# Performance work log

Hardware: AMD Instinct MI355X
Metric: run time of the kernel (lower is better)

Reference implementation:

```python
import jax, jax.numpy as jnp
import numpy as np

B, T = 256, 64
L, S = 1024, 512          # large / small LSTM cell sizes
NC = 239                  # num classes
EPS = 1e-5                # BatchNorm eps (inference mode, mean=0, var=1)
TAU = 1.0                 # gumbel-softmax temperature


def setup_inputs() -> dict:
    key = jax.random.key(0)
    ks = jax.random.split(key, 12)
    def N(i, shape, s=0.05):
        return jax.random.normal(ks[i], shape, dtype=jnp.float32) * s
    return {
        "x": N(0, (B, T, 2048), 1.0),
        "x_small": N(1, (B, T, 1280), 1.0),
        # proj_mlp: Linear(2048->2048) + BN(2048) [inference] + ReLU
        "W_p": N(2, (2048, 2048)), "b_p": jnp.zeros(2048),
        "g_p": jnp.ones(2048), "be_p": jnp.zeros(2048),
        # small_proj_mlp: Linear(1280->512) + BN(512) + ReLU
        "W_s": N(3, (512, 1280)), "b_s": jnp.zeros(512),
        "g_s": jnp.ones(512), "be_s": jnp.zeros(512),
        # large LSTMCell: input 2048+512 -> hidden L
        "Wih_l": N(4, (4 * L, 2048 + 512)), "Whh_l": N(5, (4 * L, L)),
        "bih_l": jnp.zeros(4 * L), "bhh_l": jnp.zeros(4 * L),
        # small LSTMCell: input 512 -> hidden S
        "Wih_s": N(6, (4 * S, 512)), "Whh_s": N(7, (4 * S, S)),
        "bih_s": jnp.zeros(4 * S), "bhh_s": jnp.zeros(4 * S),
        # gate linear: (512 + 2L) -> 2
        "W_g": N(8, (2, 512 + 2 * L)), "b_g": jnp.zeros(2),
        # classifier: L -> NC
        "W_c": N(9, (NC, L)), "b_c": jnp.zeros(NC),
    }


def _bn_relu(x, gamma, beta):
    # inference BatchNorm1d with running_mean=0, running_var=1
    return jax.nn.relu(x * (gamma / np.sqrt(1.0 + EPS)) + beta)


def _lstm_cell(xin, h, c, Wih, Whh, bih, bhh):
    gates = xin @ Wih.T + bih + h @ Whh.T + bhh
    i, f, g, o = jnp.split(gates, 4, axis=1)
    c2 = jax.nn.sigmoid(f) * c + jax.nn.sigmoid(i) * jnp.tanh(g)
    h2 = jax.nn.sigmoid(o) * jnp.tanh(c2)
    return h2, c2


def reference(x, x_small, W_p, b_p, g_p, be_p, W_s, b_s, g_s, be_s,
              Wih_l, Whh_l, bih_l, bhh_l, Wih_s, Whh_s, bih_s, bhh_s,
              W_g, b_g, W_c, b_c):
    # project all frames at once (time-parallel part of the net)
    feats = _bn_relu(jnp.einsum('bti,oi->bto', x, W_p) + b_p, g_p, be_p)        # [B,T,2048]
    sfeats = _bn_relu(jnp.einsum('bti,oi->bto', x_small, W_s) + b_s, g_s, be_s)  # [B,T,512]

    def step(carry, ft_st):
        h_l, c_l, h_s, c_s = carry
        f_t, s_t = ft_st                                   # [B,2048], [B,512]
        h_s2, c_s2 = _lstm_cell(s_t, h_s, c_s, Wih_s, Whh_s, bih_s, bhh_s)
        # gating on OLD large state
        p = jax.nn.log_softmax(jnp.concatenate([s_t, h_l, c_l], 1) @ W_g.T + b_g, axis=1)
        y_soft = jax.nn.softmax(p / TAU, axis=1)
        y_hard = jax.nn.one_hot(jnp.argmax(y_soft, axis=1), 2, dtype=y_soft.dtype)
        r = y_hard + y_soft - jax.lax.stop_gradient(y_soft)  # straight-through hard sample
        h_ln, c_ln = _lstm_cell(jnp.concatenate([f_t, s_t], 1), h_l, c_l,
                                Wih_l, Whh_l, bih_l, bhh_l)
        ph = jnp.concatenate([h_s2[:, :S], h_l[:, S:L]], 1)  # partial (skip) hidden
        pc = jnp.concatenate([c_s2[:, :S], c_l[:, S:L]], 1)
        h_l2 = r[:, 0:1] * h_ln + r[:, 1:2] * ph
        c_l2 = r[:, 0:1] * c_ln + r[:, 1:2] * pc
        return (h_l2, c_l2, h_s2, c_s2), r

    z_l = jnp.zeros((B, L), jnp.float32)
    z_s = jnp.zeros((B, S), jnp.float32)
    (h_l, c_l, _, _), r_stack = jax.lax.scan(
        step, (z_l, z_l, z_s, z_s),
        (feats.transpose(1, 0, 2), sfeats.transpose(1, 0, 2)))
    logits = h_l @ W_c.T + b_c                             # [B,NC]
    return logits, r_stack                                 # r_stack: [T,B,2]
```

## Files before the change

### kernel.cpp

```cpp
#include <hip/hip_runtime.h>
#include <math.h>


typedef _Float16 f16;
typedef _Float16 f16x4 __attribute__((ext_vector_type(4)));
typedef _Float16 f16x8 __attribute__((ext_vector_type(8)));
typedef float f32x4 __attribute__((ext_vector_type(4)));

__device__ __forceinline__ float sigf(float x) { return 1.0f / (1.0f + expf(-x)); }

__device__ __forceinline__ void gload16(const f16* g, f16* l) {
  __builtin_amdgcn_global_load_lds((const __attribute__((address_space(1))) void*)g,
                                   (__attribute__((address_space(3))) void*)l, 16, 0, 0);
}

__global__ __launch_bounds__(256) void pack_img(const float* __restrict__ src,
    int C, int KT, int t0, int map, f16* __restrict__ dh, f16* __restrict__ dl,
    int slots)
{
  int gid = blockIdx.x * 256 + threadIdx.x;
  if (gid >= slots) return;
  int lane = gid & 63;
  int j = (gid >> 6) & 7;
  int pk = gid >> 9;
  int p = pk / KT, kt = pk - p * KT;
  int r = p * 128 + j * 16 + (lane & 15);
  int rg = map ? (((r & 255) << 6) + t0 + (r >> 8)) : r;
  int c = kt * 32 + (lane >> 4) * 8;
  const float* s = src + (long long)rg * C + c;
  float4 v0 = *(const float4*)s, v1 = *(const float4*)(s + 4);
  f16x8 h, l;
  h[0]=(f16)v0.x; l[0]=(f16)(v0.x-(float)h[0]);
  h[1]=(f16)v0.y; l[1]=(f16)(v0.y-(float)h[1]);
  h[2]=(f16)v0.z; l[2]=(f16)(v0.z-(float)h[2]);
  h[3]=(f16)v0.w; l[3]=(f16)(v0.w-(float)h[3]);
  h[4]=(f16)v1.x; l[4]=(f16)(v1.x-(float)h[4]);
  h[5]=(f16)v1.y; l[5]=(f16)(v1.y-(float)h[5]);
  h[6]=(f16)v1.z; l[6]=(f16)(v1.z-(float)h[6]);
  h[7]=(f16)v1.w; l[7]=(f16)(v1.w-(float)h[7]);
  *(f16x8*)(dh + (long long)gid * 8) = h;
  *(f16x8*)(dl + (long long)gid * 8) = l;
}

template <int EPI>
__global__ __launch_bounds__(512, 1) void gmm256(
    const f16* __restrict__ Ah0, const f16* __restrict__ Al0, int KT0,
    const f16* __restrict__ Ah1, const f16* __restrict__ Al1, int KT1,
    const f16* __restrict__ Bh, const f16* __restrict__ Bl, int KTB,
    float* __restrict__ C, int ldc,
    f16* __restrict__ Ch, f16* __restrict__ Cl, int KTout,
    const float* __restrict__ e0, const float* __restrict__ e1,
    const float* __restrict__ e2)
{
  __shared__ __align__(16) char smem[131072];
  f16 (*sm)[4][8192] = (f16 (*)[4][8192])smem;
  const int tid = threadIdx.x;
  const int w = tid >> 6, lane = tid & 63;
  const int wr = w >> 2, wc = w & 3;
  const int fr = lane & 15, fq = lane >> 4;
  const int pA = blockIdx.y, pB = blockIdx.x;
  const int sarr = w >> 1, shalf = w & 1;

  const int nt = KT0 + KT1;

  auto stage = [&](int buf, int kt) {
    const f16* base;
    if (sarr >= 2) {
      base = ((sarr == 2) ? Bh : Bl) + ((long long)(pB * 2 + shalf) * KTB + kt) * 4096;
    } else if (kt < KT0) {
      base = ((sarr == 0) ? Ah0 : Al0) + ((long long)(pA * 2 + shalf) * KT0 + kt) * 4096;
    } else {
      base = ((sarr == 0) ? Ah1 : Al1) + ((long long)(pA * 2 + shalf) * KT1 + (kt - KT0)) * 4096;
    }
    f16* dst = &sm[buf][sarr][shalf * 4096];
#pragma unroll
    for (int j = 0; j < 8; ++j)
      gload16(base + j * 512 + lane * 8, dst + j * 512);
  };

  f32x4 acc[8][4];
#pragma unroll
  for (int m = 0; m < 8; ++m)
#pragma unroll
    for (int n = 0; n < 4; ++n) acc[m][n] = (f32x4){0.f, 0.f, 0.f, 0.f};

  stage(0, 0);
  __syncthreads();
  int cur = 0;
  for (int kt = 0; kt < nt; ++kt) {
    if (kt + 1 < nt) stage(cur ^ 1, kt + 1);
    f16x8 bh_[4], bl_[4];
#pragma unroll
    for (int n = 0; n < 4; ++n) {
      bh_[n] = *(const f16x8*)&sm[cur][2][(wc * 4 + n) * 512 + lane * 8];
      bl_[n] = *(const f16x8*)&sm[cur][3][(wc * 4 + n) * 512 + lane * 8];
    }
#pragma unroll
    for (int m = 0; m < 8; ++m) {
      f16x8 ah = *(const f16x8*)&sm[cur][0][wr * 4096 + m * 512 + lane * 8];
      f16x8 al = *(const f16x8*)&sm[cur][1][wr * 4096 + m * 512 + lane * 8];
#pragma unroll
      for (int n = 0; n < 4; ++n) {
        acc[m][n] = __builtin_amdgcn_mfma_f32_16x16x32_f16(ah, bh_[n], acc[m][n], 0, 0, 0);
        acc[m][n] = __builtin_amdgcn_mfma_f32_16x16x32_f16(ah, bl_[n], acc[m][n], 0, 0, 0);
        acc[m][n] = __builtin_amdgcn_mfma_f32_16x16x32_f16(al, bh_[n], acc[m][n], 0, 0, 0);
      }
    }
    __syncthreads();
    cur ^= 1;
  }

  if (EPI == 1) {
#pragma unroll
    for (int m = 0; m < 8; ++m) {
#pragma unroll
      for (int n = 0; n < 4; ++n) {
        const int col = pB * 256 + wc * 64 + n * 16 + fr;
        const float add = e0[col] + e1[col];
#pragma unroll
        for (int r = 0; r < 4; ++r) {
          const int row = pA * 256 + wr * 128 + m * 16 + fq * 4 + r;
          C[(long long)row * ldc + col] = acc[m][n][r] + add;
        }
      }
    }
  } else {
    float* cb = (float*)smem;
    const int CBLD = 260;
    for (int q = 0; q < 4; ++q) {
      __syncthreads();
      if (wr == (q >> 1)) {
#pragma unroll
        for (int mm = 0; mm < 4; ++mm) {
          const int m = (q & 1) * 4 + mm;
#pragma unroll
          for (int n = 0; n < 4; ++n) {
            const int colL = wc * 64 + n * 16 + fr;
            const int colG = pB * 256 + colL;
            const float p0 = e0[colG], p1 = e1[colG] * 0.99999500003750f, p2 = e2[colG];
#pragma unroll
            for (int r = 0; r < 4; ++r) {
              const int rq = mm * 16 + fq * 4 + r;
              cb[rq * CBLD + colL] = fmaxf((acc[m][n][r] + p0) * p1 + p2, 0.f);
            }
          }
        }
      }
      __syncthreads();
      const int ktl = w;
      const int p_out = pA * 2 + (q >> 1);
#pragma unroll
      for (int jp = 0; jp < 4; ++jp) {
        const int rL = jp * 16 + fr;
        const float* s = &cb[rL * CBLD + ktl * 32 + fq * 8];
        float4 v0 = *(const float4*)s, v1 = *(const float4*)(s + 4);
        float vv[8] = {v0.x, v0.y, v0.z, v0.w, v1.x, v1.y, v1.z, v1.w};
        f16x8 h, l;
#pragma unroll
        for (int e = 0; e < 8; ++e) {
          h[e] = (f16)vv[e]; l[e] = (f16)(vv[e] - (float)h[e]);
        }
        const int j_img = (q & 1) * 4 + jp;
        const long long o =
            (((long long)p_out * KTout + (pB * 8 + ktl)) * 8 + j_img) * 512 + lane * 8;
        *(f16x8*)(Ch + o) = h;
        *(f16x8*)(Cl + o) = l;
      }
    }
  }
}

__device__ __forceinline__ void gcore_step(int pA, int pB,
    const f16* __restrict__ Ah0, const f16* __restrict__ Al0, int KT0,
    const f16* __restrict__ Bh, const f16* __restrict__ Bl,
    float* __restrict__ C, int ldc, const float* __restrict__ G)
{
  __shared__ __align__(16) char smem[65536];
  f16 (*sm)[4][4096] = (f16 (*)[4][4096])smem;
  const int tid = threadIdx.x;
  const int w = tid >> 6, lane = tid & 63;
  const int wr = w >> 1, wc = w & 1;
  const int fr = lane & 15, fq = lane >> 4;

  const f16* aH = Ah0 + (long long)pA * KT0 * 4096;
  const f16* aL = Al0 + (long long)pA * KT0 * 4096;
  const f16* bH = Bh + (long long)pB * KT0 * 4096;
  const f16* bL = Bl + (long long)pB * KT0 * 4096;

  auto stage = [&](int buf, int kt) {
    const f16* src;
    if (w == 0)      src = aH + (long long)kt * 4096;
    else if (w == 1) src = aL + (long long)kt * 4096;
    else if (w == 2) src = bH + (long long)kt * 4096;
    else             src = bL + (long long)kt * 4096;
    f16* dst = &sm[buf][w][0];
#pragma unroll
    for (int j = 0; j < 8; ++j)
      gload16(src + j * 512 + lane * 8, dst + j * 512);
  };

  f32x4 acc[4][4];
#pragma unroll
  for (int m = 0; m < 4; ++m)
#pragma unroll
    for (int n = 0; n < 4; ++n) acc[m][n] = (f32x4){0.f, 0.f, 0.f, 0.f};

  stage(0, 0);
  __syncthreads();
  int cur = 0;
  for (int kt = 0; kt < KT0; ++kt) {
    if (kt + 1 < KT0) stage(cur ^ 1, kt + 1);
    f16x8 bhx[4], blx[4];
#pragma unroll
    for (int n = 0; n < 4; ++n) {
      bhx[n] = *(const f16x8*)&sm[cur][2][(wc * 4 + n) * 512 + lane * 8];
      blx[n] = *(const f16x8*)&sm[cur][3][(wc * 4 + n) * 512 + lane * 8];
    }
#pragma unroll
    for (int m = 0; m < 4; ++m) {
      f16x8 ah = *(const f16x8*)&sm[cur][0][(wr * 4 + m) * 512 + lane * 8];
      f16x8 al = *(const f16x8*)&sm[cur][1][(wr * 4 + m) * 512 + lane * 8];
#pragma unroll
      for (int n = 0; n < 4; ++n) {
        acc[m][n] = __builtin_amdgcn_mfma_f32_16x16x32_f16(ah, bhx[n], acc[m][n], 0, 0, 0);
        acc[m][n] = __builtin_amdgcn_mfma_f32_16x16x32_f16(ah, blx[n], acc[m][n], 0, 0, 0);
        acc[m][n] = __builtin_amdgcn_mfma_f32_16x16x32_f16(al, bhx[n], acc[m][n], 0, 0, 0);
      }
    }
    __syncthreads();
    cur ^= 1;
  }

#pragma unroll
  for (int m = 0; m < 4; ++m) {
#pragma unroll
    for (int n = 0; n < 4; ++n) {
      const int col = pB * 128 + wc * 64 + n * 16 + fr;
#pragma unroll
      for (int r = 0; r < 4; ++r) {
        const int row = pA * 128 + wr * 64 + m * 16 + fq * 4 + r;
        const long long idx = (long long)row * ldc + col;
        C[idx] = acc[m][n][r] + G[idx];
      }
    }
  }
}

__global__ __launch_bounds__(256) void stepg_k(
    const f16* __restrict__ hlh, const f16* __restrict__ hll,
    const f16* __restrict__ hsh, const f16* __restrict__ hsl,
    const f16* __restrict__ Whl_h, const f16* __restrict__ Whl_l,
    const f16* __restrict__ Whs_h, const f16* __restrict__ Whs_l,
    const float* __restrict__ Gl, const float* __restrict__ Gs,
    float* __restrict__ gl, float* __restrict__ gs)
{
  if (blockIdx.y < 32)
    gcore_step(blockIdx.x, blockIdx.y, hlh, hll, 32,
               Whl_h, Whl_l, gl, 4096, Gl);
  else
    gcore_step(blockIdx.x, blockIdx.y - 32, hsh, hsl, 16,
               Whs_h, Whs_l, gs, 2048, Gs);
}

__global__ __launch_bounds__(256) void zs_img_k(const f16* __restrict__ sfh,
    const f16* __restrict__ sfl, const float* __restrict__ Wg,
    float* __restrict__ zs, int t0)
{
  const int wv = threadIdx.x >> 6, lane = threadIdx.x & 63;
  const int rr = blockIdx.x * 4 + wv;
  const int p = rr >> 7, j = (rr >> 4) & 7, fr = rr & 15;
  const int kt = lane >> 2, fq = lane & 3;
  const long long a = (((long long)p * 16 + kt) * 8 + j) * 512 + (fq * 16 + fr) * 8;
  f16x8 h8 = *(const f16x8*)(sfh + a);
  f16x8 l8 = *(const f16x8*)(sfl + a);
  const int k0 = kt * 32 + fq * 8;
  float z0 = 0.f, z1 = 0.f;
#pragma unroll
  for (int i = 0; i < 8; ++i) {
    float s = (float)h8[i] + (float)l8[i];
    z0 += s * Wg[k0 + i]; z1 += s * Wg[2560 + k0 + i];
  }
#pragma unroll
  for (int off = 32; off > 0; off >>= 1) {
    z0 += __shfl_down(z0, off);
    z1 += __shfl_down(z1, off);
  }
  if (lane == 0) {
    const int bt = ((rr & 255) << 6) + t0 + (rr >> 8);
    zs[bt * 2] = z0; zs[bt * 2 + 1] = z1;
  }
}

__global__ __launch_bounds__(256) void step_upd(
    const float* __restrict__ gl, const float* __restrict__ gs,
    const float* __restrict__ hl_o, const float* __restrict__ cl_o,
    const float* __restrict__ cs_o,
    float* __restrict__ hl_n, float* __restrict__ cl_n,
    float* __restrict__ hs_n, float* __restrict__ cs_n,
    f16* __restrict__ hlIh, f16* __restrict__ hlIl,
    f16* __restrict__ hsIh, f16* __restrict__ hsIl,
    const float* __restrict__ zs, const float* __restrict__ Wg,
    const float* __restrict__ bg, float* __restrict__ rout, int t)
{
  const int b = blockIdx.x, tid = threadIdx.x;
  __shared__ float red0[256], red1[256];
  __shared__ float shs[512], scs[512];
  __shared__ float rsh[2];

  const int pb = b >> 7, jb = (b >> 4) & 7, frb = b & 15;

  float4 h4 = *(const float4*)(hl_o + (long long)b * 1024 + tid * 4);
  float4 c4 = *(const float4*)(cl_o + (long long)b * 1024 + tid * 4);
  float4 w0h = *(const float4*)(Wg + 512 + tid * 4);
  float4 w0c = *(const float4*)(Wg + 1536 + tid * 4);
  float4 w1h = *(const float4*)(Wg + 2560 + 512 + tid * 4);
  float4 w1c = *(const float4*)(Wg + 2560 + 1536 + tid * 4);
  red0[tid] = h4.x * w0h.x + h4.y * w0h.y + h4.z * w0h.z + h4.w * w0h.w
            + c4.x * w0c.x + c4.y * w0c.y + c4.z * w0c.z + c4.w * w0c.w;
  red1[tid] = h4.x * w1h.x + h4.y * w1h.y + h4.z * w1h.z + h4.w * w1h.w
            + c4.x * w1c.x + c4.y * w1c.y + c4.z * w1c.z + c4.w * w1c.w;

  {
    const float* gb = gs + (long long)b * 2048;
#pragma unroll
    for (int e = 0; e < 2; ++e) {
      const int n = tid * 2 + e;
      float gi = gb[n], gf = gb[512 + n], gg = gb[1024 + n], go = gb[1536 + n];
      float c2 = sigf(gf) * cs_o[b * 512 + n] + sigf(gi) * tanhf(gg);
      float h2 = sigf(go) * tanhf(c2);
      shs[n] = h2; scs[n] = c2;
      hs_n[b * 512 + n] = h2; cs_n[b * 512 + n] = c2;
      const int kt = n >> 5, fqn = (n >> 3) & 3, en = n & 7;
      const long long o = (((long long)pb * 16 + kt) * 8 + jb) * 512
                        + (fqn * 16 + frb) * 8 + en;
      f16 hh = (f16)h2;
      hsIh[o] = hh; hsIl[o] = (f16)(h2 - (float)hh);
    }
  }
  __syncthreads();
  for (int s = 128; s > 0; s >>= 1) {
    if (tid < s) { red0[tid] += red0[tid + s]; red1[tid] += red1[tid + s]; }
    __syncthreads();
  }
  if (tid == 0) {
    float z0 = red0[0] + zs[(b * 64 + t) * 2 + 0] + bg[0];
    float z1 = red1[0] + zs[(b * 64 + t) * 2 + 1] + bg[1];
    int hard = (z1 > z0) ? 1 : 0;
    rsh[0] = hard ? 0.0f : 1.0f; rsh[1] = hard ? 1.0f : 0.0f;
    rout[b * 2 + 0] = rsh[0]; rout[b * 2 + 1] = rsh[1];
  }
  __syncthreads();
  const float r0 = rsh[0], r1 = rsh[1];

  {
    const float* glb = gl + (long long)b * 4096;
    const int n = tid * 4;
    float4 gi4 = *(const float4*)(glb + n);
    float4 gf4 = *(const float4*)(glb + 1024 + n);
    float4 gg4 = *(const float4*)(glb + 2048 + n);
    float4 go4 = *(const float4*)(glb + 3072 + n);
    float4 co4 = *(const float4*)(cl_o + (long long)b * 1024 + n);
    float4 ho4 = *(const float4*)(hl_o + (long long)b * 1024 + n);
    float gi[4] = {gi4.x, gi4.y, gi4.z, gi4.w};
    float gf[4] = {gf4.x, gf4.y, gf4.z, gf4.w};
    float gg[4] = {gg4.x, gg4.y, gg4.z, gg4.w};
    float go[4] = {go4.x, go4.y, go4.z, go4.w};
    float co[4] = {co4.x, co4.y, co4.z, co4.w};
    float ho[4] = {ho4.x, ho4.y, ho4.z, ho4.w};
    float hv[4], cv[4];
    f16x4 ih, il;
#pragma unroll
    for (int e = 0; e < 4; ++e) {
      float cln = sigf(gf[e]) * co[e] + sigf(gi[e]) * tanhf(gg[e]);
      float hln = sigf(go[e]) * tanhf(cln);
      float ph = (n + e < 512) ? shs[n + e] : ho[e];
      float pc = (n + e < 512) ? scs[n + e] : co[e];
      hv[e] = r0 * hln + r1 * ph;
      cv[e] = r0 * cln + r1 * pc;
      ih[e] = (f16)hv[e]; il[e] = (f16)(hv[e] - (float)ih[e]);
    }
    float4 hw = {hv[0], hv[1], hv[2], hv[3]};
    float4 cw = {cv[0], cv[1], cv[2], cv[3]};
    *(float4*)(hl_n + (long long)b * 1024 + n) = hw;
    *(float4*)(cl_n + (long long)b * 1024 + n) = cw;
    const int kt = n >> 5, fqn = (n >> 3) & 3, en = n & 7;
    const long long o = (((long long)pb * 32 + kt) * 8 + jb) * 512
                      + (fqn * 16 + frb) * 8 + en;
    *(f16x4*)(hlIh + o) = ih;
    *(f16x4*)(hlIl + o) = il;
  }
}

__global__ __launch_bounds__(256) void logits_k(const float* __restrict__ hl,
                                                const float* __restrict__ Wc,
                                                const float* __restrict__ bc,
                                                float* __restrict__ out)
{
  __shared__ float hsd[1024];
  const int b = blockIdx.x, tid = threadIdx.x;
  *(float4*)(hsd + tid * 4) = *(const float4*)(hl + (long long)b * 1024 + tid * 4);
  __syncthreads();
  if (tid < 239) {
    const float* w = Wc + (long long)tid * 1024;
    float s = 0.0f;
    for (int k = 0; k < 1024; k += 4) {
      float4 wv = *(const float4*)(w + k);
      s += hsd[k] * wv.x + hsd[k + 1] * wv.y + hsd[k + 2] * wv.z + hsd[k + 3] * wv.w;
    }
    out[(long long)b * 239 + tid] = s + bc[tid];
  }
}

#define BKK 32
template <int BM, int BN, int TM, int TN, int EPI>
__global__ __launch_bounds__(256) void gemm_nt(
    int M, int N,
    const float* __restrict__ A0, long long as0, const float* __restrict__ B0, long long bs0, int K0,
    const float* __restrict__ A1, long long as1, const float* __restrict__ B1, long long bs1, int K1,
    const float* __restrict__ A2, long long as2, const float* __restrict__ B2, long long bs2, int K2,
    float* __restrict__ C, long long ldc,
    const float* __restrict__ e0, const float* __restrict__ e1, const float* __restrict__ e2)
{
  __shared__ float As[BKK][BM + 4];
  __shared__ float Bs[BKK][BN + 4];
  const int tid = threadIdx.x;
  const int m0 = blockIdx.x * BM;
  const int n0 = blockIdx.y * BN;
  constexpr int C4 = BKK / 4;
  constexpr int RPP = 256 / C4;
  constexpr int APASS = BM / RPP;
  constexpr int BPASS = BN / RPP;
  const int lr = tid / C4;
  const int lc = tid % C4;
  float4 pa[APASS], pb[BPASS];
  const int nt = (K0 + K1 + K2) / BKK;
  auto load = [&](int kt) {
    const int kg = kt * BKK;
    const float* ap; long long as_; const float* bp; long long bs_;
    if (kg < K0)           { ap = A0 + kg;          as_ = as0; bp = B0 + kg;          bs_ = bs0; }
    else if (kg < K0 + K1) { int kl = kg - K0;      ap = A1 + kl; as_ = as1; bp = B1 + kl; bs_ = bs1; }
    else                   { int kl = kg - K0 - K1; ap = A2 + kl; as_ = as2; bp = B2 + kl; bs_ = bs2; }
#pragma unroll
    for (int p = 0; p < APASS; p++) {
      int r = lr + p * RPP;
      pa[p] = *(const float4*)(ap + (long long)(m0 + r) * as_ + lc * 4);
    }
#pragma unroll
    for (int p = 0; p < BPASS; p++) {
      int r = lr + p * RPP;
      pb[p] = *(const float4*)(bp + (long long)(n0 + r) * bs_ + lc * 4);
    }
  };
  const int tx = tid % (BN / TN);
  const int ty = tid / (BN / TN);
  float acc[TM][TN];
#pragma unroll
  for (int i = 0; i < TM; i++)
#pragma unroll
    for (int j = 0; j < TN; j++) acc[i][j] = 0.0f;
  load(0);
  for (int kt = 0; kt < nt; ++kt) {
    __syncthreads();
#pragma unroll
    for (int p = 0; p < APASS; p++) {
      int r = lr + p * RPP;
      As[lc * 4 + 0][r] = pa[p].x; As[lc * 4 + 1][r] = pa[p].y;
      As[lc * 4 + 2][r] = pa[p].z; As[lc * 4 + 3][r] = pa[p].w;
    }
#pragma unroll
    for (int p = 0; p < BPASS; p++) {
      int r = lr + p * RPP;
      Bs[lc * 4 + 0][r] = pb[p].x; Bs[lc * 4 + 1][r] = pb[p].y;
      Bs[lc * 4 + 2][r] = pb[p].z; Bs[lc * 4 + 3][r] = pb[p].w;
    }
    __syncthreads();
    if (kt + 1 < nt) load(kt + 1);
#pragma unroll
    for (int k = 0; k < BKK; k++) {
      float a[TM], bfr[TN];
#pragma unroll
      for (int i = 0; i < TM; i++) a[i] = As[k][ty * TM + i];
#pragma unroll
      for (int j = 0; j < TN; j++) bfr[j] = Bs[k][tx * TN + j];
#pragma unroll
      for (int i = 0; i < TM; i++)
#pragma unroll
        for (int j = 0; j < TN; j++) acc[i][j] += a[i] * bfr[j];
    }
  }
#pragma unroll
  for (int i = 0; i < TM; i++) {
    const int m = m0 + ty * TM + i;
    const int n = n0 + tx * TN;
    float v[TN];
#pragma unroll
    for (int j = 0; j < TN; j++) {
      float a = acc[i][j];
      if (EPI == 0) {
        float s = e1[n + j] * 0.999995f;
        a = (a + e0[n + j]) * s + e2[n + j];
        a = fmaxf(a, 0.0f);
      } else {
        a = a + e0[n + j] + e1[n + j];
      }
      v[j] = a;
    }
    float4 o; o.x = v[0]; o.y = v[1]; o.z = v[2]; o.w = v[3];
    *(float4*)(C + (long long)m * ldc + n) = o;
  }
}

__global__ __launch_bounds__(256) void zs32_k(const float* __restrict__ sf,
                                              const float* __restrict__ Wg,
                                              float* __restrict__ zs)
{
  const int wave = threadIdx.x >> 6, lane = threadIdx.x & 63;
  const int row = blockIdx.x * 4 + wave;
  const float* s = sf + (long long)row * 512 + lane * 8;
  const float* w0 = Wg + lane * 8;
  const float* w1 = Wg + 2560 + lane * 8;
  float4 sa = *(const float4*)s, sb = *(const float4*)(s + 4);
  float4 a0 = *(const float4*)w0, b0 = *(const float4*)(w0 + 4);
  float4 a1 = *(const float4*)w1, b1 = *(const float4*)(w1 + 4);
  float z0 = sa.x * a0.x + sa.y * a0.y + sa.z * a0.z + sa.w * a0.w
           + sb.x * b0.x + sb.y * b0.y + sb.z * b0.z + sb.w * b0.w;
  float z1 = sa.x * a1.x + sa.y * a1.y + sa.z * a1.z + sa.w * a1.w
           + sb.x * b1.x + sb.y * b1.y + sb.z * b1.z + sb.w * b1.w;
#pragma unroll
  for (int off = 32; off > 0; off >>= 1) {
    z0 += __shfl_down(z0, off);
    z1 += __shfl_down(z1, off);
  }
  if (lane == 0) { zs[row * 2] = z0; zs[row * 2 + 1] = z1; }
}

__global__ __launch_bounds__(256) void step_upd32(
    const float* __restrict__ gl, const float* __restrict__ gs,
    const float* __restrict__ hl_o, const float* __restrict__ cl_o,
    const float* __restrict__ cs_o,
    float* __restrict__ hl_n, float* __restrict__ cl_n,
    float* __restrict__ hs_n, float* __restrict__ cs_n,
    const float* __restrict__ zs, const float* __restrict__ Wg,
    const float* __restrict__ bg, float* __restrict__ rout, int t)
{
  const int b = blockIdx.x, tid = threadIdx.x;
  __shared__ float red0[256], red1[256];
  __shared__ float shs[512], scs[512];
  __shared__ float rsh[2];
  float4 h4 = *(const float4*)(hl_o + (long long)b * 1024 + tid * 4);
  float4 c4 = *(const float4*)(cl_o + (long long)b * 1024 + tid * 4);
  float4 w0h = *(const float4*)(Wg + 512 + tid * 4);
  float4 w0c = *(const float4*)(Wg + 1536 + tid * 4);
  float4 w1h = *(const float4*)(Wg + 2560 + 512 + tid * 4);
  float4 w1c = *(const float4*)(Wg + 2560 + 1536 + tid * 4);
  red0[tid] = h4.x * w0h.x + h4.y * w0h.y + h4.z * w0h.z + h4.w * w0h.w
            + c4.x * w0c.x + c4.y * w0c.y + c4.z * w0c.z + c4.w * w0c.w;
  red1[tid] = h4.x * w1h.x + h4.y * w1h.y + h4.z * w1h.z + h4.w * w1h.w
            + c4.x * w1c.x + c4.y * w1c.y + c4.z * w1c.z + c4.w * w1c.w;
  {
    const float* gb = gs + (long long)b * 2048;
#pragma unroll
    for (int e = 0; e < 2; ++e) {
      const int n = tid * 2 + e;
      float gi = gb[n], gf = gb[512 + n], gg = gb[1024 + n], go = gb[1536 + n];
      float c2 = sigf(gf) * cs_o[b * 512 + n] + sigf(gi) * tanhf(gg);
      float h2 = sigf(go) * tanhf(c2);
      shs[n] = h2; scs[n] = c2;
      hs_n[b * 512 + n] = h2; cs_n[b * 512 + n] = c2;
    }
  }
  __syncthreads();
  for (int s = 128; s > 0; s >>= 1) {
    if (tid < s) { red0[tid] += red0[tid + s]; red1[tid] += red1[tid + s]; }
    __syncthreads();
  }
  if (tid == 0) {
    float z0 = red0[0] + zs[(b * 64 + t) * 2 + 0] + bg[0];
    float z1 = red1[0] + zs[(b * 64 + t) * 2 + 1] + bg[1];
    int hard = (z1 > z0) ? 1 : 0;
    rsh[0] = hard ? 0.0f : 1.0f; rsh[1] = hard ? 1.0f : 0.0f;
    rout[b * 2 + 0] = rsh[0]; rout[b * 2 + 1] = rsh[1];
  }
  __syncthreads();
  const float r0 = rsh[0], r1 = rsh[1];
  {
    const float* glb = gl + (long long)b * 4096;
    const int n = tid * 4;
    float4 gi4 = *(const float4*)(glb + n);
    float4 gf4 = *(const float4*)(glb + 1024 + n);
    float4 gg4 = *(const float4*)(glb + 2048 + n);
    float4 go4 = *(const float4*)(glb + 3072 + n);
    float4 co4 = *(const float4*)(cl_o + (long long)b * 1024 + n);
    float4 ho4 = *(const float4*)(hl_o + (long long)b * 1024 + n);
    float gi[4] = {gi4.x, gi4.y, gi4.z, gi4.w};
    float gf[4] = {gf4.x, gf4.y, gf4.z, gf4.w};
    float gg[4] = {gg4.x, gg4.y, gg4.z, gg4.w};
    float go[4] = {go4.x, go4.y, go4.z, go4.w};
    float co[4] = {co4.x, co4.y, co4.z, co4.w};
    float ho[4] = {ho4.x, ho4.y, ho4.z, ho4.w};
    float hv[4], cv[4];
#pragma unroll
    for (int e = 0; e < 4; ++e) {
      float cln = sigf(gf[e]) * co[e] + sigf(gi[e]) * tanhf(gg[e]);
      float hln = sigf(go[e]) * tanhf(cln);
      float ph = (n + e < 512) ? shs[n + e] : ho[e];
      float pc = (n + e < 512) ? scs[n + e] : co[e];
      hv[e] = r0 * hln + r1 * ph;
      cv[e] = r0 * cln + r1 * pc;
    }
    float4 hw = {hv[0], hv[1], hv[2], hv[3]};
    float4 cw = {cv[0], cv[1], cv[2], cv[3]};
    *(float4*)(hl_n + (long long)b * 1024 + n) = hw;
    *(float4*)(cl_n + (long long)b * 1024 + n) = cw;
  }
}

extern "C" void kernel_launch(void* const* d_in, const int* in_sizes, int n_in,
                              void* d_out, int out_size, void* d_ws, size_t ws_size,
                              hipStream_t stream)
{
  const float* x     = (const float*)d_in[0];
  const float* xs    = (const float*)d_in[1];
  const float* W_p   = (const float*)d_in[2];
  const float* b_p   = (const float*)d_in[3];
  const float* g_p   = (const float*)d_in[4];
  const float* be_p  = (const float*)d_in[5];
  const float* W_s   = (const float*)d_in[6];
  const float* b_s   = (const float*)d_in[7];
  const float* g_s   = (const float*)d_in[8];
  const float* be_s  = (const float*)d_in[9];
  const float* Wih_l = (const float*)d_in[10];
  const float* Whh_l = (const float*)d_in[11];
  const float* bih_l = (const float*)d_in[12];
  const float* bhh_l = (const float*)d_in[13];
  const float* Wih_s = (const float*)d_in[14];
  const float* Whh_s = (const float*)d_in[15];
  const float* bih_s = (const float*)d_in[16];
  const float* bhh_s = (const float*)d_in[17];
  const float* W_g   = (const float*)d_in[18];
  const float* b_g   = (const float*)d_in[19];
  const float* W_c   = (const float*)d_in[20];
  const float* b_c   = (const float*)d_in[21];
  float* out = (float*)d_out;
  float* r_out = out + 61184;

  const int BT = 16384;
  const size_t FIXEDB = 100794368ULL;
  const size_t CHUNKB = 12320768ULL;
  int Tp = 0;
  for (int T = 64; T >= 1; T >>= 1)
    if (FIXEDB + CHUNKB * (size_t)T + 65536 <= ws_size) { Tp = T; break; }

  if (Tp > 0) {
    char* base = (char*)d_ws;
    size_t off = 0;
    auto alloc = [&](size_t n) { void* p = base + off; off += (n + 255) & ~255ULL; return p; };
    f16* WpI[2]  = {(f16*)alloc(8388608),  (f16*)alloc(8388608)};
    f16* WsI[2]  = {(f16*)alloc(1310720),  (f16*)alloc(1310720)};
    f16* WilI[2] = {(f16*)alloc(20971520), (f16*)alloc(20971520)};
    f16* WisI[2] = {(f16*)alloc(2097152),  (f16*)alloc(2097152)};
    f16* WhlI[2] = {(f16*)alloc(8388608),  (f16*)alloc(8388608)};
    f16* WhsI[2] = {(f16*)alloc(2097152),  (f16*)alloc(2097152)};
    f16* hlI[2] = {(f16*)alloc(524288), (f16*)alloc(524288)};
    f16* hsI[2] = {(f16*)alloc(262144), (f16*)alloc(262144)};
    float* zs  = (float*)alloc(131072);
    float* hl[2] = {(float*)alloc(1048576), (float*)alloc(1048576)};
    float* cl[2] = {(float*)alloc(1048576), (float*)alloc(1048576)};
    float* hsb[2] = {(float*)alloc(524288), (float*)alloc(524288)};
    float* csb[2] = {(float*)alloc(524288), (float*)alloc(524288)};
    float* gates_l = (float*)alloc(4194304);
    float* gates_s = (float*)alloc(2097152);
    f16* xI[2]  = {(f16*)alloc(1048576ULL * Tp), (f16*)alloc(1048576ULL * Tp)};
    f16* xsI[2] = {(f16*)alloc(655360ULL * Tp),  (f16*)alloc(655360ULL * Tp)};
    f16* feI[2] = {(f16*)alloc(1048576ULL * Tp), (f16*)alloc(1048576ULL * Tp)};
    f16* sfI[2] = {(f16*)alloc(262144ULL * Tp),  (f16*)alloc(262144ULL * Tp)};
    float* GxlC = (float*)alloc(4194304ULL * Tp);
    float* GxsC = (float*)alloc(2097152ULL * Tp);

    pack_img<<<2048, 256, 0, stream>>>(W_p,   2048, 64, 0, 0, WpI[0],  WpI[1],  524288);
    pack_img<<<320,  256, 0, stream>>>(W_s,   1280, 40, 0, 0, WsI[0],  WsI[1],  81920);
    pack_img<<<5120, 256, 0, stream>>>(Wih_l, 2560, 80, 0, 0, WilI[0], WilI[1], 1310720);
    pack_img<<<512,  256, 0, stream>>>(Wih_s, 512,  16, 0, 0, WisI[0], WisI[1], 131072);
    pack_img<<<2048, 256, 0, stream>>>(Whh_l, 1024, 32, 0, 0, WhlI[0], WhlI[1], 524288);
    pack_img<<<512,  256, 0, stream>>>(Whh_s, 512,  16, 0, 0, WhsI[0], WhsI[1], 131072);

    hipMemsetAsync(hl[0], 0, 1048576, stream);
    hipMemsetAsync(cl[0], 0, 1048576, stream);
    hipMemsetAsync(hsb[0], 0, 524288, stream);
    hipMemsetAsync(csb[0], 0, 524288, stream);
    hipMemsetAsync(hlI[0], 0, 524288, stream);
    hipMemsetAsync(hlI[1], 0, 524288, stream);
    hipMemsetAsync(hsI[0], 0, 262144, stream);
    hipMemsetAsync(hsI[1], 0, 262144, stream);

    const int rows = 256 * Tp;
    for (int t0 = 0; t0 < 64; t0 += Tp) {
      pack_img<<<rows * 2048 / 8 / 256, 256, 0, stream>>>(
          x, 2048, 64, t0, 1, xI[0], xI[1], rows * 256);
      pack_img<<<rows * 1280 / 8 / 256, 256, 0, stream>>>(
          xs, 1280, 40, t0, 1, xsI[0], xsI[1], rows * 160);
      gmm256<0><<<dim3(2, rows / 256), 512, 0, stream>>>(
          xsI[0], xsI[1], 40, nullptr, nullptr, 0,
          WsI[0], WsI[1], 40,
          nullptr, 0, sfI[0], sfI[1], 16, b_s, g_s, be_s);
      zs_img_k<<<rows / 4, 256, 0, stream>>>(sfI[0], sfI[1], W_g, zs, t0);
      gmm256<0><<<dim3(8, rows / 256), 512, 0, stream>>>(
          xI[0], xI[1], 64, nullptr, nullptr, 0,
          WpI[0], WpI[1], 64,
          nullptr, 0, feI[0], feI[1], 64, b_p, g_p, be_p);
      gmm256<1><<<dim3(16, rows / 256), 512, 0, stream>>>(
          feI[0], feI[1], 64, sfI[0], sfI[1], 16,
          WilI[0], WilI[1], 80,
          GxlC, 4096, nullptr, nullptr, 0, bih_l, bhh_l, nullptr);
      gmm256<1><<<dim3(8, rows / 256), 512, 0, stream>>>(
          sfI[0], sfI[1], 16, nullptr, nullptr, 0,
          WisI[0], WisI[1], 16,
          GxsC, 2048, nullptr, nullptr, 0, bih_s, bhh_s, nullptr);

      for (int tt = 0; tt < Tp; ++tt) {
        const int t = t0 + tt;
        const int o = t & 1, nw = o ^ 1;
        stepg_k<<<dim3(2, 48), 256, 0, stream>>>(
            hlI[0], hlI[1], hsI[0], hsI[1],
            WhlI[0], WhlI[1], WhsI[0], WhsI[1],
            GxlC + (long long)tt * 256 * 4096, GxsC + (long long)tt * 256 * 2048,
            gates_l, gates_s);
        step_upd<<<256, 256, 0, stream>>>(
            gates_l, gates_s, hl[o], cl[o], csb[o],
            hl[nw], cl[nw], hsb[nw], csb[nw],
            hlI[0], hlI[1], hsI[0], hsI[1],
            zs, W_g, b_g, r_out + (long long)t * 512, t);
      }
    }
    logits_k<<<256, 256, 0, stream>>>(hl[0], W_c, b_c, out);
    return;
  }

  float* ws = (float*)d_ws;
  size_t offf = 0;
  auto allocf = [&](size_t n) { float* p = ws + offf; offf += n; return p; };
  float* feats   = allocf((size_t)BT * 2048);
  float* sfeats  = allocf((size_t)BT * 512);
  float* zs      = allocf((size_t)BT * 2);
  float* gates_l = allocf((size_t)256 * 4096);
  float* gates_s = allocf((size_t)256 * 2048);
  float* hl[2] = { allocf(256 * 1024), allocf(256 * 1024) };
  float* cl[2] = { allocf(256 * 1024), allocf(256 * 1024) };
  float* hsb[2] = { allocf(256 * 512),  allocf(256 * 512) };
  float* csb[2] = { allocf(256 * 512),  allocf(256 * 512) };

  hipMemsetAsync(hl[0], 0, 256 * 1024 * sizeof(float), stream);
  hipMemsetAsync(cl[0], 0, 256 * 1024 * sizeof(float), stream);
  hipMemsetAsync(hsb[0], 0, 256 * 512 * sizeof(float), stream);
  hipMemsetAsync(csb[0], 0, 256 * 512 * sizeof(float), stream);

  gemm_nt<128, 64, 8, 4, 0><<<dim3(BT / 128, 2048 / 64), 256, 0, stream>>>(
      BT, 2048, x, 2048, W_p, 2048, 2048,
      nullptr, 0, nullptr, 0, 0, nullptr, 0, nullptr, 0, 0,
      feats, 2048, b_p, g_p, be_p);
  gemm_nt<128, 64, 8, 4, 0><<<dim3(BT / 128, 512 / 64), 256, 0, stream>>>(
      BT, 512, xs, 1280, W_s, 1280, 1280,
      nullptr, 0, nullptr, 0, 0, nullptr, 0, nullptr, 0, 0,
      sfeats, 512, b_s, g_s, be_s);
  zs32_k<<<BT / 4, 256, 0, stream>>>(sfeats, W_g, zs);

  for (int t = 0; t < 64; ++t) {
    const int o = t & 1, nw = o ^ 1;
    gemm_nt<64, 64, 4, 4, 1><<<dim3(4, 2048 / 64), 256, 0, stream>>>(
        256, 2048, sfeats + (long long)t * 512, 64LL * 512, Wih_s, 512, 512,
        hsb[o], 512, Whh_s, 512, 512, nullptr, 0, nullptr, 0, 0,
        gates_s, 2048, bih_s, bhh_s, nullptr);
    gemm_nt<64, 64, 4, 4, 1><<<dim3(4, 4096 / 64), 256, 0, stream>>>(
        256, 4096, feats + (long long)t * 2048, 64LL * 2048, Wih_l, 2560, 2048,
        sfeats + (long long)t * 512, 64LL * 512, Wih_l + 2048, 2560, 512,
        hl[o], 1024, Whh_l, 1024, 1024,
        gates_l, 4096, bih_l, bhh_l, nullptr);
    step_upd32<<<256, 256, 0, stream>>>(
        gates_l, gates_s, hl[o], cl[o], csb[o],
        hl[nw], cl[nw], hsb[nw], csb[nw],
        zs, W_g, b_g, r_out + (long long)t * 512, t);
  }
  logits_k<<<256, 256, 0, stream>>>(hl[0], W_c, b_c, out);
}
```

Measured before the change: 3.954 ms.

## Unify GEMM kernels into templated core with smaller M tiles and XCD-aware swizzle

Replaces the fixed 256x256 GEMM and the separate recurrent-step GEMM with one templated core that uses 128-row tiles and a configurable N width (128 or 256). The intent is more blocks per launch to fill the GPU, with a block-index swizzle so neighbouring blocks that share B panels land on the same XCD for better L2 reuse. The same core serves the per-step recurrent GEMM with an add-G epilogue. Smaller tiles lower the arithmetic intensity per block and re-read A more often.

```diff
diff --git a/kernel.cpp b/kernel.cpp
--- a/kernel.cpp
+++ b/kernel.cpp
@@ -42,63 +42,87 @@
   *(f16x8*)(dl + (long long)gid * 8) = l;
 }
 
-template <int EPI>
-__global__ __launch_bounds__(512, 1) void gmm256(
+template <int BN, int EPI>
+__device__ __forceinline__ void gcore(
+    int pA, int pB,
     const f16* __restrict__ Ah0, const f16* __restrict__ Al0, int KT0,
     const f16* __restrict__ Ah1, const f16* __restrict__ Al1, int KT1,
     const f16* __restrict__ Bh, const f16* __restrict__ Bl, int KTB,
-    float* __restrict__ C, int ldc,
+    float* __restrict__ C, int ldc, const float* __restrict__ G,
     f16* __restrict__ Ch, f16* __restrict__ Cl, int KTout,
     const float* __restrict__ e0, const float* __restrict__ e1,
     const float* __restrict__ e2)
 {
-  __shared__ __align__(16) char smem[131072];
-  f16 (*sm)[4][8192] = (f16 (*)[4][8192])smem;
+  constexpr int WAVES = BN / 32;
+  constexpr int WN = BN / 64;
+  constexpr int NBU = BN / 16;
+  constexpr int U = 16 + BN / 8;
+  constexpr int NU = U / WAVES;
+  __shared__ __align__(16) f16 smem[2][U * 512];
+
   const int tid = threadIdx.x;
   const int w = tid >> 6, lane = tid & 63;
-  const int wr = w >> 2, wc = w & 3;
+  const int wr = w / WN, wc = w % WN;
   const int fr = lane & 15, fq = lane >> 4;
-  const int pA = blockIdx.y, pB = blockIdx.x;
-  const int sarr = w >> 1, shalf = w & 1;
-
   const int nt = KT0 + KT1;
 
-  auto stage = [&](int buf, int kt) {
-    const f16* base;
-    if (sarr >= 2) {
-      base = ((sarr == 2) ? Bh : Bl) + ((long long)(pB * 2 + shalf) * KTB + kt) * 4096;
-    } else if (kt < KT0) {
-      base = ((sarr == 0) ? Ah0 : Al0) + ((long long)(pA * 2 + shalf) * KT0 + kt) * 4096;
-    } else {
-      base = ((sarr == 0) ? Ah1 : Al1) + ((long long)(pA * 2 + shalf) * KT1 + (kt - KT0)) * 4096;
-    }
-    f16* dst = &sm[buf][sarr][shalf * 4096];
-#pragma unroll
-    for (int j = 0; j < 8; ++j)
-      gload16(base + j * 512 + lane * 8, dst + j * 512);
+  const f16* up[NU];
+  auto setptrs = [&](int kt) {
+#pragma unroll
+    for (int i = 0; i < NU; ++i) {
+      const int u = w * NU + i;
+      const f16* src;
+      if (u < 16) {
+        const int j = u & 7;
+        const f16* AH = Ah0; const f16* AL = Al0; int KT = KT0, ktl = kt;
+        if (KT1 > 0 && kt >= KT0) { AH = Ah1; AL = Al1; KT = KT1; ktl = kt - KT0; }
+        src = ((u < 8) ? AH : AL) + (((long long)pA * KT + ktl) * 8 + j) * 512;
+      } else {
+        const int j = u - 16;
+        const f16* IMG = (j < NBU) ? Bh : Bl;
+        const int jb = (j < NBU) ? j : j - NBU;
+        const int panel = pB * (BN / 128) + (jb >> 3);
+        src = IMG + (((long long)panel * KTB + kt) * 8 + (jb & 7)) * 512;
+      }
+      up[i] = src + lane * 8;
+    }
   };
-
-  f32x4 acc[8][4];
-#pragma unroll
-  for (int m = 0; m < 8; ++m)
+  auto stage = [&](int buf) {
+#pragma unroll
+    for (int i = 0; i < NU; ++i) {
+      gload16(up[i], &smem[buf][(w * NU + i) * 512]);
+      up[i] += 4096;
+    }
+  };
+
+  f32x4 acc[4][4];
+#pragma unroll
+  for (int m = 0; m < 4; ++m)
 #pragma unroll
     for (int n = 0; n < 4; ++n) acc[m][n] = (f32x4){0.f, 0.f, 0.f, 0.f};
 
-  stage(0, 0);
+  setptrs(0);
+  stage(0);
   __syncthreads();
   int cur = 0;
   for (int kt = 0; kt < nt; ++kt) {
-    if (kt + 1 < nt) stage(cur ^ 1, kt + 1);
+    if (kt + 1 < nt) {
+      if (KT1 > 0 && kt + 1 == KT0) setptrs(kt + 1);
+      stage(cur ^ 1);
+    }
+    const f16* sb = smem[cur];
     f16x8 bh_[4], bl_[4];
 #pragma unroll
     for (int n = 0; n < 4; ++n) {
-      bh_[n] = *(const f16x8*)&sm[cur][2][(wc * 4 + n) * 512 + lane * 8];
-      bl_[n] = *(const f16x8*)&sm[cur][3][(wc * 4 + n) * 512 + lane * 8];
-    }
-#pragma unroll
-    for (int m = 0; m < 8; ++m) {
-      f16x8 ah = *(const f16x8*)&sm[cur][0][wr * 4096 + m * 512 + lane * 8];
-      f16x8 al = *(const f16x8*)&sm[cur][1][wr * 4096 + m * 512 + lane * 8];
+      const int jb = wc * 4 + n;
+      bh_[n] = *(const f16x8*)&sb[(16 + jb) * 512 + lane * 8];
+      bl_[n] = *(const f16x8*)&sb[(16 + NBU + jb) * 512 + lane * 8];
+    }
+#pragma unroll
+    for (int m = 0; m < 4; ++m) {
+      const int ja = wr * 4 + m;
+      f16x8 ah = *(const f16x8*)&sb[ja * 512 + lane * 8];
+      f16x8 al = *(const f16x8*)&sb[(8 + ja) * 512 + lane * 8];
 #pragma unroll
       for (int n = 0; n < 4; ++n) {
         acc[m][n] = __builtin_amdgcn_mfma_f32_16x16x32_f16(ah, bh_[n], acc[m][n], 0, 0, 0);
@@ -110,156 +134,116 @@
     cur ^= 1;
   }
 
-  if (EPI == 1) {
-#pragma unroll
-    for (int m = 0; m < 8; ++m) {
+  if constexpr (EPI == 1 || EPI == 2) {
+#pragma unroll
+    for (int m = 0; m < 4; ++m) {
 #pragma unroll
       for (int n = 0; n < 4; ++n) {
-        const int col = pB * 256 + wc * 64 + n * 16 + fr;
-        const float add = e0[col] + e1[col];
+        const int col = pB * BN + wc * 64 + n * 16 + fr;
+        const float add = (EPI == 1) ? (e0[col] + e1[col]) : 0.f;
 #pragma unroll
         for (int r = 0; r < 4; ++r) {
-          const int row = pA * 256 + wr * 128 + m * 16 + fq * 4 + r;
-          C[(long long)row * ldc + col] = acc[m][n][r] + add;
+          const int row = pA * 128 + wr * 64 + m * 16 + fq * 4 + r;
+          const long long idx = (long long)row * ldc + col;
+          float v = acc[m][n][r] + add;
+          if (EPI == 2) v += G[idx];
+          C[idx] = v;
         }
       }
     }
   } else {
     float* cb = (float*)smem;
-    const int CBLD = 260;
-    for (int q = 0; q < 4; ++q) {
-      __syncthreads();
-      if (wr == (q >> 1)) {
-#pragma unroll
-        for (int mm = 0; mm < 4; ++mm) {
-          const int m = (q & 1) * 4 + mm;
+    const int CBLD = 132;
+    for (int h = 0; h < 2; ++h) {
+      if (wr == h) {
+#pragma unroll
+        for (int m = 0; m < 4; ++m) {
 #pragma unroll
           for (int n = 0; n < 4; ++n) {
             const int colL = wc * 64 + n * 16 + fr;
-            const int colG = pB * 256 + colL;
-            const float p0 = e0[colG], p1 = e1[colG] * 0.99999500003750f, p2 = e2[colG];
+            const int colG = pB * 128 + colL;
+            const float p0 = e0[colG], p1 = e1[colG] * 0.99999500003750f,
+                        p2 = e2[colG];
 #pragma unroll
             for (int r = 0; r < 4; ++r) {
-              const int rq = mm * 16 + fq * 4 + r;
+              const int rq = m * 16 + fq * 4 + r;
               cb[rq * CBLD + colL] = fmaxf((acc[m][n][r] + p0) * p1 + p2, 0.f);
             }
           }
         }
       }
       __syncthreads();
-      const int ktl = w;
-      const int p_out = pA * 2 + (q >> 1);
-#pragma unroll
-      for (int jp = 0; jp < 4; ++jp) {
-        const int rL = jp * 16 + fr;
-        const float* s = &cb[rL * CBLD + ktl * 32 + fq * 8];
+#pragma unroll
+      for (int jl = 0; jl < 4; ++jl) {
+        const float* s = &cb[(jl * 16 + fr) * CBLD + w * 32 + fq * 8];
         float4 v0 = *(const float4*)s, v1 = *(const float4*)(s + 4);
         float vv[8] = {v0.x, v0.y, v0.z, v0.w, v1.x, v1.y, v1.z, v1.w};
-        f16x8 h, l;
+        f16x8 hh, ll;
 #pragma unroll
         for (int e = 0; e < 8; ++e) {
-          h[e] = (f16)vv[e]; l[e] = (f16)(vv[e] - (float)h[e]);
+          hh[e] = (f16)vv[e]; ll[e] = (f16)(vv[e] - (float)hh[e]);
         }
-        const int j_img = (q & 1) * 4 + jp;
         const long long o =
-            (((long long)p_out * KTout + (pB * 8 + ktl)) * 8 + j_img) * 512 + lane * 8;
-        *(f16x8*)(Ch + o) = h;
-        *(f16x8*)(Cl + o) = l;
+            (((long long)pA * KTout + pB * 4 + w) * 8 + (h * 4 + jl)) * 512
+            + lane * 8;
+        *(f16x8*)(Ch + o) = hh;
+        *(f16x8*)(Cl + o) = ll;
       }
-    }
-  }
-}
-
-__device__ __forceinline__ void gcore_step(int pA, int pB,
+      __syncthreads();
+    }
+  }
+}
+
+template <int BN, int EPI>
+__global__ __launch_bounds__(BN * 2) void gmm_k(
+    int gB, int swz,
     const f16* __restrict__ Ah0, const f16* __restrict__ Al0, int KT0,
-    const f16* __restrict__ Bh, const f16* __restrict__ Bl,
-    float* __restrict__ C, int ldc, const float* __restrict__ G)
-{
-  __shared__ __align__(16) char smem[65536];
-  f16 (*sm)[4][4096] = (f16 (*)[4][4096])smem;
-  const int tid = threadIdx.x;
-  const int w = tid >> 6, lane = tid & 63;
-  const int wr = w >> 1, wc = w & 1;
-  const int fr = lane & 15, fq = lane >> 4;
-
-  const f16* aH = Ah0 + (long long)pA * KT0 * 4096;
-  const f16* aL = Al0 + (long long)pA * KT0 * 4096;
-  const f16* bH = Bh + (long long)pB * KT0 * 4096;
-  const f16* bL = Bl + (long long)pB * KT0 * 4096;
-
-  auto stage = [&](int buf, int kt) {
-    const f16* src;
-    if (w == 0)      src = aH + (long long)kt * 4096;
-    else if (w == 1) src = aL + (long long)kt * 4096;
-    else if (w == 2) src = bH + (long long)kt * 4096;
-    else             src = bL + (long long)kt * 4096;
-    f16* dst = &sm[buf][w][0];
-#pragma unroll
-    for (int j = 0; j < 8; ++j)
-      gload16(src + j * 512 + lane * 8, dst + j * 512);
-  };
-
-  f32x4 acc[4][4];
-#pragma unroll
-  for (int m = 0; m < 4; ++m)
-#pragma unroll
-    for (int n = 0; n < 4; ++n) acc[m][n] = (f32x4){0.f, 0.f, 0.f, 0.f};
-
-  stage(0, 0);
-  __syncthreads();
-  int cur = 0;
-  for (int kt = 0; kt < KT0; ++kt) {
-    if (kt + 1 < KT0) stage(cur ^ 1, kt + 1);
-    f16x8 bhx[4], blx[4];
-#pragma unroll
-    for (int n = 0; n < 4; ++n) {
-      bhx[n] = *(const f16x8*)&sm[cur][2][(wc * 4 + n) * 512 + lane * 8];
-      blx[n] = *(const f16x8*)&sm[cur][3][(wc * 4 + n) * 512 + lane * 8];
-    }
-#pragma unroll
-    for (int m = 0; m < 4; ++m) {
-      f16x8 ah = *(const f16x8*)&sm[cur][0][(wr * 4 + m) * 512 + lane * 8];
-      f16x8 al = *(const f16x8*)&sm[cur][1][(wr * 4 + m) * 512 + lane * 8];
-#pragma unroll
-      for (int n = 0; n < 4; ++n) {
-        acc[m][n] = __builtin_amdgcn_mfma_f32_16x16x32_f16(ah, bhx[n], acc[m][n], 0, 0, 0);
-        acc[m][n] = __builtin_amdgcn_mfma_f32_16x16x32_f16(ah, blx[n], acc[m][n], 0, 0, 0);
-        acc[m][n] = __builtin_amdgcn_mfma_f32_16x16x32_f16(al, bhx[n], acc[m][n], 0, 0, 0);
-      }
-    }
-    __syncthreads();
-    cur ^= 1;
-  }
-
-#pragma unroll
-  for (int m = 0; m < 4; ++m) {
-#pragma unroll
-    for (int n = 0; n < 4; ++n) {
-      const int col = pB * 128 + wc * 64 + n * 16 + fr;
-#pragma unroll
-      for (int r = 0; r < 4; ++r) {
-        const int row = pA * 128 + wr * 64 + m * 16 + fq * 4 + r;
-        const long long idx = (long long)row * ldc + col;
-        C[idx] = acc[m][n][r] + G[idx];
-      }
-    }
-  }
+    const f16* __restrict__ Ah1, const f16* __restrict__ Al1, int KT1,
+    const f16* __restrict__ Bh, const f16* __restrict__ Bl, int KTB,
+    float* __restrict__ C, int ldc, const float* __restrict__ G,
+    f16* __restrict__ Ch, f16* __restrict__ Cl, int KTout,
+    const float* __restrict__ e0, const float* __restrict__ e1,
+    const float* __restrict__ e2)
+{
+  const int lin = blockIdx.x;
+  int pA, pB;
+  if (swz) {
+    const int xc = lin & 7, j = lin >> 3, cpx = gB >> 3;
+    pB = xc * cpx + (j % cpx);
+    pA = j / cpx;
+  } else {
+    pB = lin % gB;
+    pA = lin / gB;
+  }
+  gcore<BN, EPI>(pA, pB, Ah0, Al0, KT0, Ah1, Al1, KT1, Bh, Bl, KTB,
+                 C, ldc, G, Ch, Cl, KTout, e0, e1, e2);
 }
 
 __global__ __launch_bounds__(256) void stepg_k(
     const f16* __restrict__ hlh, const f16* __restrict__ hll,
     const f16* __restrict__ hsh, const f16* __restrict__ hsl,
-    const f16* __restrict__ Whl_h, const f16* __restrict__ Whl_l,
-    const f16* __restrict__ Whs_h, const f16* __restrict__ Whs_l,
+    const f16* __restrict__ Whlh, const f16* __restrict__ Whll,
+    const f16* __restrict__ Whsh, const f16* __restrict__ Whsl,
     const float* __restrict__ Gl, const float* __restrict__ Gs,
     float* __restrict__ gl, float* __restrict__ gs)
 {
-  if (blockIdx.y < 32)
-    gcore_step(blockIdx.x, blockIdx.y, hlh, hll, 32,
-               Whl_h, Whl_l, gl, 4096, Gl);
-  else
-    gcore_step(blockIdx.x, blockIdx.y - 32, hsh, hsl, 16,
-               Whs_h, Whs_l, gs, 2048, Gs);
+  const int lin = blockIdx.x;
+  const int xc = lin & 7, j = lin >> 3;
+  const f16 *Ah, *Al, *Bh, *Bl;
+  const float* G; float* C;
+  int KT, ldc, pA, pB;
+  if (j < 8) {
+    pA = j >> 2; pB = xc * 4 + (j & 3);
+    Ah = hlh; Al = hll; Bh = Whlh; Bl = Whll; KT = 32; ldc = 4096;
+    C = gl; G = Gl;
+  } else {
+    const int jj = j - 8;
+    pA = jj >> 1; pB = xc * 2 + (jj & 1);
+    Ah = hsh; Al = hsl; Bh = Whsh; Bl = Whsl; KT = 16; ldc = 2048;
+    C = gs; G = Gs;
+  }
+  gcore<128, 2>(pA, pB, Ah, Al, KT, nullptr, nullptr, 0, Bh, Bl, KT,
+                C, ldc, G, nullptr, nullptr, 0, nullptr, nullptr, nullptr);
 }
 
 __global__ __launch_bounds__(256) void zs_img_k(const f16* __restrict__ sfh,
@@ -694,33 +678,38 @@
     hipMemsetAsync(hsI[1], 0, 262144, stream);
 
     const int rows = 256 * Tp;
+    const int gA = rows / 128;
     for (int t0 = 0; t0 < 64; t0 += Tp) {
       pack_img<<<rows * 2048 / 8 / 256, 256, 0, stream>>>(
           x, 2048, 64, t0, 1, xI[0], xI[1], rows * 256);
       pack_img<<<rows * 1280 / 8 / 256, 256, 0, stream>>>(
           xs, 1280, 40, t0, 1, xsI[0], xsI[1], rows * 160);
-      gmm256<0><<<dim3(2, rows / 256), 512, 0, stream>>>(
+      gmm_k<128, 0><<<gA * 4, 256, 0, stream>>>(
+          4, 0,
           xsI[0], xsI[1], 40, nullptr, nullptr, 0,
           WsI[0], WsI[1], 40,
-          nullptr, 0, sfI[0], sfI[1], 16, b_s, g_s, be_s);
+          nullptr, 0, nullptr, sfI[0], sfI[1], 16, b_s, g_s, be_s);
       zs_img_k<<<rows / 4, 256, 0, stream>>>(sfI[0], sfI[1], W_g, zs, t0);
-      gmm256<0><<<dim3(8, rows / 256), 512, 0, stream>>>(
+      gmm_k<128, 0><<<gA * 16, 256, 0, stream>>>(
+          16, 1,
           xI[0], xI[1], 64, nullptr, nullptr, 0,
           WpI[0], WpI[1], 64,
-          nullptr, 0, feI[0], feI[1], 64, b_p, g_p, be_p);
-      gmm256<1><<<dim3(16, rows / 256), 512, 0, stream>>>(
+          nullptr, 0, nullptr, feI[0], feI[1], 64, b_p, g_p, be_p);
+      gmm_k<256, 1><<<gA * 16, 512, 0, stream>>>(
+          16, 1,
           feI[0], feI[1], 64, sfI[0], sfI[1], 16,
           WilI[0], WilI[1], 80,
-          GxlC, 4096, nullptr, nullptr, 0, bih_l, bhh_l, nullptr);
-      gmm256<1><<<dim3(8, rows / 256), 512, 0, stream>>>(
+          GxlC, 4096, nullptr, nullptr, nullptr, 0, bih_l, bhh_l, nullptr);
+      gmm_k<128, 1><<<gA * 16, 256, 0, stream>>>(
+          16, 1,
           sfI[0], sfI[1], 16, nullptr, nullptr, 0,
           WisI[0], WisI[1], 16,
-          GxsC, 2048, nullptr, nullptr, 0, bih_s, bhh_s, nullptr);
+          GxsC, 2048, nullptr, nullptr, nullptr, 0, bih_s, bhh_s, nullptr);
 
       for (int tt = 0; tt < Tp; ++tt) {
         const int t = t0 + tt;
         const int o = t & 1, nw = o ^ 1;
-        stepg_k<<<dim3(2, 48), 256, 0, stream>>>(
+        stepg_k<<<96, 256, 0, stream>>>(
             hlI[0], hlI[1], hsI[0], hsI[1],
             WhlI[0], WhlI[1], WhsI[0], WhsI[1],
             GxlC + (long long)tt * 256 * 4096, GxsC + (long long)tt * 256 * 2048,
```

After: 4.094 ms. 3.5% more time.
